# Kernel tuning notes

Hardware: AMD Instinct MI355X
Metric: run time of the kernel (lower is better)

The kernel has to match this reference:

```python
import jax, jax.numpy as jnp
import numpy as np

N = 200000
D = 128
B = 8
VS = 0.4
XMIN, YMIN, ZMIN = -50.0, -50.0, -5.0
NX, NY, NZ = 250, 250, 20
VXYZ = NX * NY * NZ
FILL = np.int32(2_000_000_000)  # > any real voxel key, so padded uniques sort last
BN_EPS = 1e-5


def _bn(x, g, b, m, v):
    # BatchNorm1d in eval mode with given running stats
    return (x - m) * jax.lax.rsqrt(v + BN_EPS) * g + b


def _leaky(x):
    return jnp.where(x >= 0, x, 0.1 * x)


def setup_inputs() -> dict:
    key = jax.random.key(0)
    ks = jax.random.split(key, 12)
    points_feature = jax.random.normal(ks[0], (N, D), jnp.float32)
    u = jax.random.uniform(ks[1], (N, 3), jnp.float32)
    lo = jnp.array([XMIN, YMIN, ZMIN], jnp.float32)
    ext = jnp.array([100.0, 100.0, 8.0], jnp.float32)
    points_center = lo + 0.001 + u * (ext - 0.002)  # strictly inside pc_range
    batch_idx = jax.random.randint(ks[2], (N,), 0, B, jnp.int32)
    foreground_mask = jax.random.randint(ks[3], (N,), 0, 2, jnp.int32).astype(bool)
    timestamp = jax.random.normal(ks[4], (B,), jnp.float32) * 0.1
    w_pf = jax.random.normal(ks[5], (3 * D, D), jnp.float32) / np.sqrt(3 * D)
    b_pf = jax.random.normal(ks[6], (D,), jnp.float32) * 0.01
    g_pf = jax.random.uniform(ks[7], (D,), jnp.float32) + 0.5
    be_pf = jax.random.normal(ks[8], (D,), jnp.float32) * 0.1
    m_pf = jax.random.normal(ks[9], (D,), jnp.float32) * 0.1
    v_pf = jax.random.uniform(ks[10], (D,), jnp.float32) + 0.5
    ks2 = jax.random.split(ks[11], 6)
    w_cp = jax.random.normal(ks2[0], (D, D), jnp.float32) / np.sqrt(D)
    b_cp = jax.random.normal(ks2[1], (D,), jnp.float32) * 0.01
    g_cp = jax.random.uniform(ks2[2], (D,), jnp.float32) + 0.5
    be_cp = jax.random.normal(ks2[3], (D,), jnp.float32) * 0.1
    m_cp = jax.random.normal(ks2[4], (D,), jnp.float32) * 0.1
    v_cp = jax.random.uniform(ks2[5], (D,), jnp.float32) + 0.5
    return dict(points_feature=points_feature, points_center=points_center,
                batch_idx=batch_idx, foreground_mask=foreground_mask,
                timestamp=timestamp,
                w_pf=w_pf, b_pf=b_pf, g_pf=g_pf, be_pf=be_pf, m_pf=m_pf, v_pf=v_pf,
                w_cp=w_cp, b_cp=b_cp, g_cp=g_cp, be_cp=be_cp, m_cp=m_cp, v_cp=v_cp)


def reference(points_feature, points_center, batch_idx, foreground_mask, timestamp,
              w_pf, b_pf, g_pf, be_pf, m_pf, v_pf,
              w_cp, b_cp, g_cp, be_cp, m_cp, v_cp):
    # NOTE: the original forward computes a time position embedding and then
    # overwrites it with zeros_like, so its net contribution is exactly zero.
    n = points_feature.shape[0]
    # voxelize point centers -> (b, xi, yi, zi) encoded as a single int key
    xi = jnp.floor((points_center[:, 0] - XMIN) / VS).astype(jnp.int32)
    yi = jnp.floor((points_center[:, 1] - YMIN) / VS).astype(jnp.int32)
    zi = jnp.floor((points_center[:, 2] - ZMIN) / VS).astype(jnp.int32)
    vkey = ((batch_idx.astype(jnp.int32) * NX + xi) * NY + yi) * NZ + zi
    # torch.unique(dim=0) sorts lexicographically == sorted scalar keys
    uk, inv = jnp.unique(vkey, return_inverse=True, size=n, fill_value=FILL)
    fgf = foreground_mask.astype(points_feature.dtype)
    # K = points_cluster_idx_fore.max() + 1 (number of foreground clusters)
    K = jnp.max(jnp.where(foreground_mask, inv, -1)) + 1
    # scatter_mean of foreground point features per cluster (empty -> 0)
    cnt = jax.ops.segment_sum(fgf, inv, num_segments=n)
    csum = jax.ops.segment_sum(points_feature * fgf[:, None], inv, num_segments=n)
    cmean = csum / jnp.maximum(cnt, 1.0)[:, None]
    proj = _leaky(_bn(cmean @ w_cp + b_cp, g_cp, be_cp, m_cp, v_cp))
    valid = jnp.arange(n) < K
    # cluster_feature_all: rows < K hold projected cluster features, rest are 0
    cfa = jnp.where(valid[:, None], proj, 0.0)
    # associate voxels: halve the batch id (agent pairing), re-unique
    akey = (uk // VXYZ // 2) * VXYZ + uk % VXYZ
    _, ainv = jnp.unique(akey, return_inverse=True, size=n, fill_value=FILL)
    # scatter_mean of cluster features over associate voxels (only valid clusters)
    acnt = jax.ops.segment_sum(valid.astype(points_feature.dtype), ainv, num_segments=n)
    asum = jax.ops.segment_sum(cfa, ainv, num_segments=n)
    amean = asum / jnp.maximum(acnt, 1.0)[:, None]
    pf_assoc = amean[ainv[inv]]   # gather per point via voxel -> associate id
    pf_clu = cfa[inv]             # gather per point cluster feature
    amask = (pf_clu - pf_assoc).sum(axis=1) > 0
    cat = jnp.concatenate([points_feature, pf_clu, pf_assoc], axis=1)
    h = _leaky(_bn(cat @ w_pf + b_pf, g_pf, be_pf, m_pf, v_pf))
    newf = jnp.where(amask[:, None], h, points_feature)
    # original early-returns points_feature if associate_mask.sum() <= 1
    return jnp.where(amask.sum() > 1, newf, points_feature)
```

## Files before the change

### kernel.cpp

```cpp
#include <hip/hip_runtime.h>

#define SCAN_BS 256
#define SCAN_IT 16
#define SCAN_CHUNK (SCAN_BS * SCAN_IT)
#define NVOX 10000000
#define NAVOX 5000000
#define NWORDS1 312500
#define NWORDS2 156250
#define VXYZK 1250000

__device__ __forceinline__ float leakyf(float x) { return x >= 0.0f ? x : 0.1f * x; }

__device__ __forceinline__ int fg_get(const void* fgp, int i, int mode) {
  return mode ? (((const unsigned char*)fgp)[i] != 0) : (((const int*)fgp)[i] != 0);
}

__global__ void k_vkey(const float* __restrict__ pc, const int* __restrict__ bidx,
                       const unsigned* __restrict__ fgw, int nw,
                       int* __restrict__ vkey, unsigned* __restrict__ bits,
                       int* __restrict__ c, int N) {
  int i = blockIdx.x * blockDim.x + threadIdx.x;
  if (i < nw && fgw[i] > 1u) atomicOr(&c[4], 1);
  if (i >= N) return;
  float x = pc[3 * i], y = pc[3 * i + 1], z = pc[3 * i + 2];
  int xi = (int)floorf((x - (-50.0f)) / 0.4f);
  int yi = (int)floorf((y - (-50.0f)) / 0.4f);
  int zi = (int)floorf((z - (-5.0f)) / 0.4f);
  xi = min(max(xi, 0), 249); yi = min(max(yi, 0), 249); zi = min(max(zi, 0), 19);
  int b = min(max(bidx[i], 0), 7);
  int key = ((b * 250 + xi) * 250 + yi) * 20 + zi;
  vkey[i] = key;
  atomicOr(&bits[key >> 5], 1u << (key & 31));
}

__global__ void k_scan_pop(const unsigned* __restrict__ bits, int nwords,
                           unsigned* __restrict__ wordpfx, unsigned* __restrict__ bsums) {
  __shared__ unsigned s[SCAN_BS];
  int tid = threadIdx.x;
  long base = (long)blockIdx.x * SCAN_CHUNK + (long)tid * SCAN_IT;
  unsigned v[SCAN_IT];
  unsigned tsum = 0;
#pragma unroll
  for (int j = 0; j < SCAN_IT; ++j) {
    long idx = base + j;
    v[j] = (idx < (long)nwords) ? (unsigned)__popc(bits[idx]) : 0u;
    tsum += v[j];
  }
  unsigned x = tsum;
  s[tid] = x;
  for (int off = 1; off < SCAN_BS; off <<= 1) {
    __syncthreads();
    unsigned y = (tid >= off) ? s[tid - off] : 0u;
    __syncthreads();
    x += y;
    s[tid] = x;
  }
  if (tid == SCAN_BS - 1) bsums[blockIdx.x] = x;
  unsigned run = x - tsum;
#pragma unroll
  for (int j = 0; j < SCAN_IT; ++j) {
    long idx = base + j;
    if (idx < (long)nwords) { wordpfx[idx] = run; run += v[j]; }
  }
}

__global__ void k_scan_sums(unsigned* __restrict__ data, int n, int* __restrict__ totalOut) {
  __shared__ unsigned s[SCAN_BS];
  int tid = threadIdx.x;
  int base = tid * SCAN_IT;
  unsigned v[SCAN_IT];
  unsigned tsum = 0;
#pragma unroll
  for (int j = 0; j < SCAN_IT; ++j) {
    int idx = base + j;
    v[j] = (idx < n) ? data[idx] : 0u;
    tsum += v[j];
  }
  unsigned x = tsum;
  s[tid] = x;
  for (int off = 1; off < SCAN_BS; off <<= 1) {
    __syncthreads();
    unsigned y = (tid >= off) ? s[tid - off] : 0u;
    __syncthreads();
    x += y;
    s[tid] = x;
  }
  if (tid == SCAN_BS - 1) *totalOut = (int)x;
  unsigned run = x - tsum;
#pragma unroll
  for (int j = 0; j < SCAN_IT; ++j) {
    int idx = base + j;
    if (idx < n) { data[idx] = run; run += v[j]; }
  }
}

__device__ __forceinline__ int rank_of(int key, const unsigned* bits,
                                       const unsigned* wordpfx, const unsigned* bsums) {
  int w = key >> 5, b = key & 31;
  return (int)(wordpfx[w] + bsums[w >> 12] + (unsigned)__popc(bits[w] & ((1u << b) - 1u)));
}

__global__ void k_inv_ukey(const int* __restrict__ vkey, const unsigned* __restrict__ bits,
                           const unsigned* __restrict__ wordpfx, const unsigned* __restrict__ bsums,
                           const void* __restrict__ fgp, int* __restrict__ inv,
                           int* __restrict__ ukey, int* __restrict__ c, int N) {
  int i = blockIdx.x * blockDim.x + threadIdx.x;
  bool valid = i < N;
  int mode = c[4];
  int r = 0;
  if (valid) {
    int k = vkey[i];
    r = rank_of(k, bits, wordpfx, bsums);
    inv[i] = r;
    ukey[r] = k;
  }
  int fgr = (valid && fg_get(fgp, i, mode)) ? r : -1;
  for (int off = 32; off > 0; off >>= 1) fgr = max(fgr, __shfl_down(fgr, off));
  if ((threadIdx.x & 63) == 0 && fgr >= 0) atomicMax(&c[2], fgr + 1);
}

__global__ void k_akey_mark(const int* __restrict__ ukey, int* __restrict__ akey,
                            unsigned* __restrict__ abits, const int* __restrict__ c, int N) {
  int r = blockIdx.x * blockDim.x + threadIdx.x;
  if (r >= N || r >= c[0]) return;
  int uk = ukey[r];
  int ak = (uk / VXYZK / 2) * VXYZK + uk % VXYZK;
  akey[r] = ak;
  atomicOr(&abits[ak >> 5], 1u << (ak & 31));
}

__global__ void k_ainv(const int* __restrict__ akey, const unsigned* __restrict__ abits,
                       const unsigned* __restrict__ awordpfx, const unsigned* __restrict__ bsums,
                       int* __restrict__ ainv, unsigned* __restrict__ gcnt,
                       const int* __restrict__ c, int N) {
  int r = blockIdx.x * blockDim.x + threadIdx.x;
  if (r >= N || r >= c[0]) return;
  int g = rank_of(akey[r], abits, awordpfx, bsums);
  ainv[r] = g;
  atomicAdd(&gcnt[g], 1u);
}

__global__ void k_build_lists(const int* __restrict__ ainv_u, const unsigned* __restrict__ gcnt,
                              int* __restrict__ mlist, int* __restrict__ nlist,
                              unsigned char* __restrict__ needp, int* __restrict__ c, int N) {
  int r = blockIdx.x * blockDim.x + threadIdx.x;
  if (r >= N || r >= c[0]) return;
  if (gcnt[ainv_u[r]] >= 2u) {
    int mp = atomicAdd(&c[5], 1);
    mlist[mp] = r;
    if (r < c[2]) {
      needp[r] = 1;
      int np = atomicAdd(&c[6], 1);
      nlist[np] = r;
    }
  }
}

__global__ void k_zero_filter(const int* __restrict__ mlist, const int* __restrict__ ainv_u,
                              const void* __restrict__ fgp, const int* __restrict__ inv,
                              const unsigned char* __restrict__ needp,
                              float* __restrict__ csum, float* __restrict__ asum,
                              float* __restrict__ cnt, int* __restrict__ clist,
                              int* __restrict__ c, int N) {
  int stride = gridDim.x * blockDim.x;
  int tid0 = blockIdx.x * blockDim.x + threadIdx.x;
  int K = c[2];
  int totalA = c[5] * 128;
  for (int idx = tid0; idx < totalA; idx += stride) {
    int r = mlist[idx >> 7];
    int d = idx & 127;
    asum[(size_t)ainv_u[r] * 128 + d] = 0.0f;
    if (r < K) csum[(size_t)r * 128 + d] = 0.0f;
  }
  int mode = c[4];
  for (int i = tid0; i < N; i += stride) {
    if (!fg_get(fgp, i, mode)) continue;
    int r = inv[i];
    if (!needp[r]) continue;
    atomicAdd(&cnt[r], 1.0f);
    int p = atomicAdd(&c[7], 1);
    clist[p] = i;
  }
}

__global__ void k_csum_accum(const float* __restrict__ pf, const int* __restrict__ clist,
                             const int* __restrict__ inv, float* __restrict__ csum,
                             const int* __restrict__ c) {
  int total = c[7] * 128;
  int stride = gridDim.x * blockDim.x;
  for (int idx = blockIdx.x * blockDim.x + threadIdx.x; idx < total; idx += stride) {
    int i = clist[idx >> 7];
    int d = idx & 127;
    atomicAdd(&csum[(size_t)inv[i] * 128 + d], pf[(size_t)i * 128 + d]);
  }
}

__global__ __launch_bounds__(128) void k_proj16(
    float* __restrict__ cs, const float* __restrict__ cnt, const int* __restrict__ nlist,
    const float* __restrict__ W, const float* __restrict__ bb,
    const float* __restrict__ gg, const float* __restrict__ be,
    const float* __restrict__ mm, const float* __restrict__ vv, const int* __restrict__ c) {
  int nc = c[6];
  int ntiles = (nc + 15) >> 4;
  __shared__ __align__(16) float tile[16][128];
  __shared__ int srow[16];
  int d = threadIdx.x;
  for (int tb = blockIdx.x; tb < ntiles; tb += gridDim.x) {
    int base = tb * 16;
    if (d < 16) srow[d] = (base + d < nc) ? nlist[base + d] : -1;
    __syncthreads();
    for (int p = 0; p < 16; ++p) {
      int r = srow[p];
      tile[p][d] = (r >= 0) ? cs[(size_t)r * 128 + d] / fmaxf(cnt[r], 1.0f) : 0.0f;
    }
    __syncthreads();
    float acc[16];
#pragma unroll
    for (int p = 0; p < 16; ++p) acc[p] = 0.0f;
    for (int k4 = 0; k4 < 32; ++k4) {
      float w0 = W[(4 * k4 + 0) * 128 + d];
      float w1 = W[(4 * k4 + 1) * 128 + d];
      float w2 = W[(4 * k4 + 2) * 128 + d];
      float w3 = W[(4 * k4 + 3) * 128 + d];
#pragma unroll
      for (int p = 0; p < 16; ++p) {
        float4 t4 = *(const float4*)&tile[p][4 * k4];
        acc[p] = fmaf(t4.x, w0, acc[p]);
        acc[p] = fmaf(t4.y, w1, acc[p]);
        acc[p] = fmaf(t4.z, w2, acc[p]);
        acc[p] = fmaf(t4.w, w3, acc[p]);
      }
    }
    float biasd = bb[d], scale = gg[d] / sqrtf(vv[d] + 1e-5f), md = mm[d], bed = be[d];
    for (int p = 0; p < 16; ++p) {
      int r = srow[p];
      if (r >= 0) {
        float pre = acc[p] + biasd;
        cs[(size_t)r * 128 + d] = leakyf((pre - md) * scale + bed);
      }
    }
    __syncthreads();
  }
}

__global__ void k_asum_accum(const float* __restrict__ cs, const int* __restrict__ nlist,
                             const int* __restrict__ ainv_u, float* __restrict__ asum,
                             float* __restrict__ acnt, const int* __restrict__ c) {
  int total = c[6] * 128;
  int stride = gridDim.x * blockDim.x;
  for (int idx = blockIdx.x * blockDim.x + threadIdx.x; idx < total; idx += stride) {
    int r = nlist[idx >> 7];
    int d = idx & 127;
    int g = ainv_u[r];
    atomicAdd(&asum[(size_t)g * 128 + d], cs[(size_t)r * 128 + d]);
    if (d == 0) atomicAdd(&acnt[g], 1.0f);
  }
}

__global__ void k_amask2(const float* __restrict__ cs, const float* __restrict__ asum,
                         const float* __restrict__ acnt, const int* __restrict__ ainv_u,
                         const int* __restrict__ mlist, const int* __restrict__ c,
                         unsigned* __restrict__ flag) {
  int mcount = c[5];
  int groups = gridDim.x * (blockDim.x >> 6);
  int j0 = blockIdx.x * (blockDim.x >> 6) + (threadIdx.x >> 6);
  int lane = threadIdx.x & 63;
  int K = c[2];
  for (int j = j0; j < mcount; j += groups) {
    int r = mlist[j];
    int g = ainv_u[r];
    float mc = fmaxf(acnt[g], 1.0f);
    bool valid = r < K;
    size_t rb = (size_t)r * 128, gb = (size_t)g * 128;
    float c0 = valid ? cs[rb + lane] : 0.0f;
    float c1 = valid ? cs[rb + 64 + lane] : 0.0f;
    float s = (c0 - asum[gb + lane] / mc) + (c1 - asum[gb + 64 + lane] / mc);
    for (int off = 32; off > 0; off >>= 1) s += __shfl_down(s, off);
    if (lane == 0) flag[r] = (s > 0.0f) ? 1u : 0u;
  }
}

__global__ void k_plist(const int* __restrict__ inv, const unsigned* __restrict__ flag,
                        int* __restrict__ plist, int* __restrict__ c, int N) {
  int i = blockIdx.x * blockDim.x + threadIdx.x;
  bool pred = (i < N) && (flag[inv[i]] != 0u);
  unsigned long long m = __ballot(pred);
  int lane = threadIdx.x & 63;
  int cnt = __popcll(m);
  int base = 0;
  if (lane == 0 && cnt) base = atomicAdd(&c[3], cnt);
  base = __shfl(base, 0);
  if (pred) plist[base + __popcll(m & ((1ull << lane) - 1ull))] = i;
}

__global__ __launch_bounds__(128) void k_fgemm(
    const float* __restrict__ pf, const float* __restrict__ cs,
    const float* __restrict__ asum, const float* __restrict__ acnt,
    const int* __restrict__ inv, const int* __restrict__ ainv_u,
    const int* __restrict__ plist, const int* __restrict__ c,
    const float* __restrict__ W, const float* __restrict__ bb,
    const float* __restrict__ gg, const float* __restrict__ be,
    const float* __restrict__ mm, const float* __restrict__ vv,
    float* __restrict__ out) {
  int pcnt = c[3];
  if (pcnt <= 1) return;
  int K = c[2];
  int ntiles = (pcnt + 15) >> 4;
  __shared__ __align__(16) float tile[16][384];
  __shared__ int si[16], sr[16], sg[16];
  __shared__ float smc[16];
  int t = threadIdx.x;
  for (int tb = blockIdx.x; tb < ntiles; tb += gridDim.x) {
    int base = tb * 16;
    if (t < 16) {
      int i = (base + t < pcnt) ? plist[base + t] : -1;
      si[t] = i;
      int r = (i >= 0) ? inv[i] : 0;
      sr[t] = r;
      int g = ainv_u[r];
      sg[t] = g;
      smc[t] = fmaxf(acnt[g], 1.0f);
    }
    __syncthreads();
    for (int e = t; e < 16 * 96; e += 128) {
      int p = e / 96, f4 = e % 96;
      int i = si[p];
      float4 v = make_float4(0.f, 0.f, 0.f, 0.f);
      if (i >= 0) {
        if (f4 < 32) {
          v = ((const float4*)pf)[(size_t)i * 32 + f4];
        } else if (f4 < 64) {
          int r = sr[p];
          if (r < K) v = ((const float4*)cs)[(size_t)r * 32 + (f4 - 32)];
        } else {
          float4 a = ((const float4*)asum)[(size_t)sg[p] * 32 + (f4 - 64)];
          float mc = smc[p];
          v = make_float4(a.x / mc, a.y / mc, a.z / mc, a.w / mc);
        }
      }
      *(float4*)&tile[p][f4 * 4] = v;
    }
    __syncthreads();
    float acc[16];
#pragma unroll
    for (int p = 0; p < 16; ++p) acc[p] = 0.0f;
    for (int k4 = 0; k4 < 96; ++k4) {
      float w0 = W[(4 * k4 + 0) * 128 + t];
      float w1 = W[(4 * k4 + 1) * 128 + t];
      float w2 = W[(4 * k4 + 2) * 128 + t];
      float w3 = W[(4 * k4 + 3) * 128 + t];
#pragma unroll
      for (int p = 0; p < 16; ++p) {
        float4 t4 = *(const float4*)&tile[p][4 * k4];
        acc[p] = fmaf(t4.x, w0, acc[p]);
        acc[p] = fmaf(t4.y, w1, acc[p]);
        acc[p] = fmaf(t4.z, w2, acc[p]);
        acc[p] = fmaf(t4.w, w3, acc[p]);
      }
    }
    float biasd = bb[t], scale = gg[t] / sqrtf(vv[t] + 1e-5f), md = mm[t], bed = be[t];
    for (int p = 0; p < 16; ++p) {
      int i = si[p];
      if (i >= 0) {
        float pre = acc[p] + biasd;
        out[(size_t)i * 128 + t] = leakyf((pre - md) * scale + bed);
      }
    }
    __syncthreads();
  }
}

extern "C" void kernel_launch(void* const* d_in, const int* in_sizes, int n_in,
                              void* d_out, int out_size, void* d_ws, size_t ws_size,
                              hipStream_t stream) {
  (void)n_in; (void)out_size; (void)ws_size;
  const float* pf   = (const float*)d_in[0];
  const float* pc   = (const float*)d_in[1];
  const int*   bidx = (const int*)d_in[2];
  const void*  fgp  = d_in[3];
  const float* Wpf  = (const float*)d_in[5];
  const float* bpf  = (const float*)d_in[6];
  const float* gpf  = (const float*)d_in[7];
  const float* bepf = (const float*)d_in[8];
  const float* mpf  = (const float*)d_in[9];
  const float* vpf  = (const float*)d_in[10];
  const float* Wcp  = (const float*)d_in[11];
  const float* bcp  = (const float*)d_in[12];
  const float* gcp  = (const float*)d_in[13];
  const float* becp = (const float*)d_in[14];
  const float* mcp  = (const float*)d_in[15];
  const float* vcp  = (const float*)d_in[16];
  float* out = (float*)d_out;
  int N = in_sizes[0] / 128;

  char* ws = (char*)d_ws;
  size_t o = 0;
  auto take = [&](size_t bytes) -> void* {
    void* p = ws + o;
    o += (bytes + 255) & ~(size_t)255;
    return p;
  };
  unsigned* bits   = (unsigned*)take((size_t)NWORDS1 * 4);
  unsigned* abits  = (unsigned*)take((size_t)NWORDS2 * 4);
  float* cnt       = (float*)take((size_t)N * 4);
  float* acnt      = (float*)take((size_t)N * 4);
  unsigned* flag   = (unsigned*)take((size_t)N * 4);
  unsigned* gcnt   = (unsigned*)take((size_t)N * 4);
  unsigned char* needp = (unsigned char*)take((size_t)N);
  int* ctr         = (int*)take(256);
  size_t zeroBytes = o;
  unsigned* wordpfx  = (unsigned*)take((size_t)NWORDS1 * 4);
  unsigned* awordpfx = (unsigned*)take((size_t)NWORDS2 * 4);
  unsigned* bsums1 = (unsigned*)take((size_t)4096 * 4);
  unsigned* bsums2 = (unsigned*)take((size_t)4096 * 4);
  int* vkey        = (int*)take((size_t)N * 4);
  int* inv         = (int*)take((size_t)N * 4);
  int* ukey        = (int*)take((size_t)N * 4);
  int* akey        = (int*)take((size_t)N * 4);
  int* ainv_u      = (int*)take((size_t)N * 4);
  int* nlist       = (int*)take((size_t)N * 4);
  int* clist       = (int*)take((size_t)N * 4);
  float* csum      = (float*)take((size_t)N * 128 * 4);
  float* asum      = (float*)take((size_t)N * 128 * 4);
  int* mlist = vkey;
  int* plist = akey;

  hipMemcpyAsync(out, pf, (size_t)N * 128 * sizeof(float),
                 hipMemcpyDeviceToDevice, stream);

  hipMemsetAsync(ws, 0, zeroBytes, stream);

  int nb = (N + 255) / 256;
  int nw = N / 4;
  k_vkey<<<nb, 256, 0, stream>>>(pc, bidx, (const unsigned*)fgp, nw, vkey, bits, ctr, N);

  int blk1 = (NWORDS1 + SCAN_CHUNK - 1) / SCAN_CHUNK;
  k_scan_pop<<<blk1, SCAN_BS, 0, stream>>>(bits, NWORDS1, wordpfx, bsums1);
  k_scan_sums<<<1, SCAN_BS, 0, stream>>>(bsums1, blk1, &ctr[0]);
  k_inv_ukey<<<nb, 256, 0, stream>>>(vkey, bits, wordpfx, bsums1, fgp, inv, ukey, ctr, N);

  k_akey_mark<<<nb, 256, 0, stream>>>(ukey, akey, abits, ctr, N);
  int blk2 = (NWORDS2 + SCAN_CHUNK - 1) / SCAN_CHUNK;
  k_scan_pop<<<blk2, SCAN_BS, 0, stream>>>(abits, NWORDS2, awordpfx, bsums2);
  k_scan_sums<<<1, SCAN_BS, 0, stream>>>(bsums2, blk2, &ctr[1]);
  k_ainv<<<nb, 256, 0, stream>>>(akey, abits, awordpfx, bsums2, ainv_u, gcnt, ctr, N);

  k_build_lists<<<nb, 256, 0, stream>>>(ainv_u, gcnt, mlist, nlist, needp, ctr, N);
  k_zero_filter<<<1024, 256, 0, stream>>>(mlist, ainv_u, fgp, inv, needp,
                                          csum, asum, cnt, clist, ctr, N);
  k_csum_accum<<<1024, 256, 0, stream>>>(pf, clist, inv, csum, ctr);
  k_proj16<<<512, 128, 0, stream>>>(csum, cnt, nlist, Wcp, bcp, gcp, becp, mcp, vcp, ctr);
  k_asum_accum<<<512, 256, 0, stream>>>(csum, nlist, ainv_u, asum, acnt, ctr);
  k_amask2<<<512, 256, 0, stream>>>(csum, asum, acnt, ainv_u, mlist, ctr, flag);

  k_plist<<<nb, 256, 0, stream>>>(inv, flag, plist, ctr, N);
  k_fgemm<<<1024, 128, 0, stream>>>(pf, csum, asum, acnt, inv, ainv_u, plist, ctr,
                                    Wpf, bpf, gpf, bepf, mpf, vpf, out);
}
```

Baseline: 467.6 us.

## Fuse all pipeline kernels into one cooperative persistent kernel with grid syncs

Replaces the chain of about fifteen kernel launches, the memset and the device-to-device memcpy with a single cooperative kernel. The phases are separated by grid-wide syncs, and the zeroing and feature copy are done by grid-stride loops inside it. This is meant to remove per-launch overhead and idle gaps between the many small dependent kernels. The cost is that every phase now runs on a fixed grid of at most 1024 blocks, grid-sync barriers are added, and the GEMM blocks move to 256 threads with 8 rows per thread-half.

```diff
diff --git a/kernel.cpp b/kernel.cpp
--- a/kernel.cpp
+++ b/kernel.cpp
@@ -1,4 +1,7 @@
 #include <hip/hip_runtime.h>
+#include <hip/hip_cooperative_groups.h>
+
+namespace cg = cooperative_groups;
 
 #define SCAN_BS 256
 #define SCAN_IT 16
@@ -8,6 +11,27 @@
 #define NWORDS1 312500
 #define NWORDS2 156250
 #define VXYZK 1250000
+#define BLK1 ((NWORDS1 + SCAN_CHUNK - 1) / SCAN_CHUNK)
+#define BLK2 ((NWORDS2 + SCAN_CHUNK - 1) / SCAN_CHUNK)
+
+struct Params {
+  const float* pf; const float* pc; const int* bidx; const void* fgp;
+  const float* Wpf; const float* bpf; const float* gpf; const float* bepf;
+  const float* mpf; const float* vpf;
+  const float* Wcp; const float* bcp; const float* gcp; const float* becp;
+  const float* mcp; const float* vcp;
+  float* out;
+  unsigned* bits; unsigned* abits; float* cnt; float* acnt;
+  unsigned* flag; unsigned* gcnt; unsigned char* needp; int* ctr;
+  unsigned* wordpfx; unsigned* awordpfx; unsigned* bsums1; unsigned* bsums2;
+  int* vkey;
+  int* inv; int* ukey;
+  int* akey;
+  int* ainv_u; int* nlist; int* clist;
+  float* csum; float* asum;
+  uint4* zbase; int zwords;
+  int N;
+};
 
 __device__ __forceinline__ float leakyf(float x) { return x >= 0.0f ? x : 0.1f * x; }
 
@@ -15,27 +39,19 @@
   return mode ? (((const unsigned char*)fgp)[i] != 0) : (((const int*)fgp)[i] != 0);
 }
 
-__global__ void k_vkey(const float* __restrict__ pc, const int* __restrict__ bidx,
-                       const unsigned* __restrict__ fgw, int nw,
-                       int* __restrict__ vkey, unsigned* __restrict__ bits,
-                       int* __restrict__ c, int N) {
-  int i = blockIdx.x * blockDim.x + threadIdx.x;
-  if (i < nw && fgw[i] > 1u) atomicOr(&c[4], 1);
-  if (i >= N) return;
-  float x = pc[3 * i], y = pc[3 * i + 1], z = pc[3 * i + 2];
-  int xi = (int)floorf((x - (-50.0f)) / 0.4f);
-  int yi = (int)floorf((y - (-50.0f)) / 0.4f);
-  int zi = (int)floorf((z - (-5.0f)) / 0.4f);
-  xi = min(max(xi, 0), 249); yi = min(max(yi, 0), 249); zi = min(max(zi, 0), 19);
-  int b = min(max(bidx[i], 0), 7);
-  int key = ((b * 250 + xi) * 250 + yi) * 20 + zi;
-  vkey[i] = key;
-  atomicOr(&bits[key >> 5], 1u << (key & 31));
-}
-
-__global__ void k_scan_pop(const unsigned* __restrict__ bits, int nwords,
-                           unsigned* __restrict__ wordpfx, unsigned* __restrict__ bsums) {
-  __shared__ unsigned s[SCAN_BS];
+__device__ __forceinline__ int rank_of(int key, const unsigned* bits,
+                                       const unsigned* wordpfx, const unsigned* bsums) {
+  int w = key >> 5, b = key & 31;
+  return (int)(wordpfx[w] + bsums[w >> 12] + (unsigned)__popc(bits[w] & ((1u << b) - 1u)));
+}
+
+struct ProjSM { float tile[16][128]; int srow[16]; };
+struct GemSM  { float tile[16][384]; int si[16]; int sr[16]; int sg[16]; float smc[16]; };
+union SM { unsigned scan[SCAN_BS]; ProjSM proj; GemSM gem; };
+
+__device__ void scan_pop_phase(const unsigned* __restrict__ bits, int nwords,
+                               unsigned* __restrict__ wordpfx, unsigned* __restrict__ bsums,
+                               unsigned* s) {
   int tid = threadIdx.x;
   long base = (long)blockIdx.x * SCAN_CHUNK + (long)tid * SCAN_IT;
   unsigned v[SCAN_IT];
@@ -64,8 +80,7 @@
   }
 }
 
-__global__ void k_scan_sums(unsigned* __restrict__ data, int n, int* __restrict__ totalOut) {
-  __shared__ unsigned s[SCAN_BS];
+__device__ void scan_sums_phase(unsigned* __restrict__ data, int n, int* totalOut, unsigned* s) {
   int tid = threadIdx.x;
   int base = tid * SCAN_IT;
   unsigned v[SCAN_IT];
@@ -94,279 +109,308 @@
   }
 }
 
-__device__ __forceinline__ int rank_of(int key, const unsigned* bits,
-                                       const unsigned* wordpfx, const unsigned* bsums) {
-  int w = key >> 5, b = key & 31;
-  return (int)(wordpfx[w] + bsums[w >> 12] + (unsigned)__popc(bits[w] & ((1u << b) - 1u)));
-}
-
-__global__ void k_inv_ukey(const int* __restrict__ vkey, const unsigned* __restrict__ bits,
-                           const unsigned* __restrict__ wordpfx, const unsigned* __restrict__ bsums,
-                           const void* __restrict__ fgp, int* __restrict__ inv,
-                           int* __restrict__ ukey, int* __restrict__ c, int N) {
-  int i = blockIdx.x * blockDim.x + threadIdx.x;
-  bool valid = i < N;
-  int mode = c[4];
-  int r = 0;
-  if (valid) {
-    int k = vkey[i];
-    r = rank_of(k, bits, wordpfx, bsums);
-    inv[i] = r;
-    ukey[r] = k;
-  }
-  int fgr = (valid && fg_get(fgp, i, mode)) ? r : -1;
-  for (int off = 32; off > 0; off >>= 1) fgr = max(fgr, __shfl_down(fgr, off));
-  if ((threadIdx.x & 63) == 0 && fgr >= 0) atomicMax(&c[2], fgr + 1);
-}
-
-__global__ void k_akey_mark(const int* __restrict__ ukey, int* __restrict__ akey,
-                            unsigned* __restrict__ abits, const int* __restrict__ c, int N) {
-  int r = blockIdx.x * blockDim.x + threadIdx.x;
-  if (r >= N || r >= c[0]) return;
-  int uk = ukey[r];
-  int ak = (uk / VXYZK / 2) * VXYZK + uk % VXYZK;
-  akey[r] = ak;
-  atomicOr(&abits[ak >> 5], 1u << (ak & 31));
-}
-
-__global__ void k_ainv(const int* __restrict__ akey, const unsigned* __restrict__ abits,
-                       const unsigned* __restrict__ awordpfx, const unsigned* __restrict__ bsums,
-                       int* __restrict__ ainv, unsigned* __restrict__ gcnt,
-                       const int* __restrict__ c, int N) {
-  int r = blockIdx.x * blockDim.x + threadIdx.x;
-  if (r >= N || r >= c[0]) return;
-  int g = rank_of(akey[r], abits, awordpfx, bsums);
-  ainv[r] = g;
-  atomicAdd(&gcnt[g], 1u);
-}
-
-__global__ void k_build_lists(const int* __restrict__ ainv_u, const unsigned* __restrict__ gcnt,
-                              int* __restrict__ mlist, int* __restrict__ nlist,
-                              unsigned char* __restrict__ needp, int* __restrict__ c, int N) {
-  int r = blockIdx.x * blockDim.x + threadIdx.x;
-  if (r >= N || r >= c[0]) return;
-  if (gcnt[ainv_u[r]] >= 2u) {
-    int mp = atomicAdd(&c[5], 1);
-    mlist[mp] = r;
-    if (r < c[2]) {
-      needp[r] = 1;
-      int np = atomicAdd(&c[6], 1);
-      nlist[np] = r;
-    }
-  }
-}
-
-__global__ void k_zero_filter(const int* __restrict__ mlist, const int* __restrict__ ainv_u,
-                              const void* __restrict__ fgp, const int* __restrict__ inv,
-                              const unsigned char* __restrict__ needp,
-                              float* __restrict__ csum, float* __restrict__ asum,
-                              float* __restrict__ cnt, int* __restrict__ clist,
-                              int* __restrict__ c, int N) {
-  int stride = gridDim.x * blockDim.x;
-  int tid0 = blockIdx.x * blockDim.x + threadIdx.x;
-  int K = c[2];
-  int totalA = c[5] * 128;
-  for (int idx = tid0; idx < totalA; idx += stride) {
-    int r = mlist[idx >> 7];
-    int d = idx & 127;
-    asum[(size_t)ainv_u[r] * 128 + d] = 0.0f;
-    if (r < K) csum[(size_t)r * 128 + d] = 0.0f;
-  }
-  int mode = c[4];
-  for (int i = tid0; i < N; i += stride) {
-    if (!fg_get(fgp, i, mode)) continue;
-    int r = inv[i];
-    if (!needp[r]) continue;
-    atomicAdd(&cnt[r], 1.0f);
-    int p = atomicAdd(&c[7], 1);
-    clist[p] = i;
-  }
-}
-
-__global__ void k_csum_accum(const float* __restrict__ pf, const int* __restrict__ clist,
-                             const int* __restrict__ inv, float* __restrict__ csum,
-                             const int* __restrict__ c) {
-  int total = c[7] * 128;
-  int stride = gridDim.x * blockDim.x;
-  for (int idx = blockIdx.x * blockDim.x + threadIdx.x; idx < total; idx += stride) {
-    int i = clist[idx >> 7];
-    int d = idx & 127;
-    atomicAdd(&csum[(size_t)inv[i] * 128 + d], pf[(size_t)i * 128 + d]);
-  }
-}
-
-__global__ __launch_bounds__(128) void k_proj16(
-    float* __restrict__ cs, const float* __restrict__ cnt, const int* __restrict__ nlist,
-    const float* __restrict__ W, const float* __restrict__ bb,
-    const float* __restrict__ gg, const float* __restrict__ be,
-    const float* __restrict__ mm, const float* __restrict__ vv, const int* __restrict__ c) {
-  int nc = c[6];
-  int ntiles = (nc + 15) >> 4;
-  __shared__ __align__(16) float tile[16][128];
-  __shared__ int srow[16];
-  int d = threadIdx.x;
-  for (int tb = blockIdx.x; tb < ntiles; tb += gridDim.x) {
-    int base = tb * 16;
-    if (d < 16) srow[d] = (base + d < nc) ? nlist[base + d] : -1;
-    __syncthreads();
-    for (int p = 0; p < 16; ++p) {
-      int r = srow[p];
-      tile[p][d] = (r >= 0) ? cs[(size_t)r * 128 + d] / fmaxf(cnt[r], 1.0f) : 0.0f;
-    }
-    __syncthreads();
-    float acc[16];
-#pragma unroll
-    for (int p = 0; p < 16; ++p) acc[p] = 0.0f;
-    for (int k4 = 0; k4 < 32; ++k4) {
-      float w0 = W[(4 * k4 + 0) * 128 + d];
-      float w1 = W[(4 * k4 + 1) * 128 + d];
-      float w2 = W[(4 * k4 + 2) * 128 + d];
-      float w3 = W[(4 * k4 + 3) * 128 + d];
-#pragma unroll
-      for (int p = 0; p < 16; ++p) {
-        float4 t4 = *(const float4*)&tile[p][4 * k4];
-        acc[p] = fmaf(t4.x, w0, acc[p]);
-        acc[p] = fmaf(t4.y, w1, acc[p]);
-        acc[p] = fmaf(t4.z, w2, acc[p]);
-        acc[p] = fmaf(t4.w, w3, acc[p]);
-      }
-    }
-    float biasd = bb[d], scale = gg[d] / sqrtf(vv[d] + 1e-5f), md = mm[d], bed = be[d];
-    for (int p = 0; p < 16; ++p) {
-      int r = srow[p];
-      if (r >= 0) {
-        float pre = acc[p] + biasd;
-        cs[(size_t)r * 128 + d] = leakyf((pre - md) * scale + bed);
-      }
-    }
-    __syncthreads();
-  }
-}
-
-__global__ void k_asum_accum(const float* __restrict__ cs, const int* __restrict__ nlist,
-                             const int* __restrict__ ainv_u, float* __restrict__ asum,
-                             float* __restrict__ acnt, const int* __restrict__ c) {
-  int total = c[6] * 128;
-  int stride = gridDim.x * blockDim.x;
-  for (int idx = blockIdx.x * blockDim.x + threadIdx.x; idx < total; idx += stride) {
-    int r = nlist[idx >> 7];
-    int d = idx & 127;
-    int g = ainv_u[r];
-    atomicAdd(&asum[(size_t)g * 128 + d], cs[(size_t)r * 128 + d]);
-    if (d == 0) atomicAdd(&acnt[g], 1.0f);
-  }
-}
-
-__global__ void k_amask2(const float* __restrict__ cs, const float* __restrict__ asum,
-                         const float* __restrict__ acnt, const int* __restrict__ ainv_u,
-                         const int* __restrict__ mlist, const int* __restrict__ c,
-                         unsigned* __restrict__ flag) {
-  int mcount = c[5];
-  int groups = gridDim.x * (blockDim.x >> 6);
-  int j0 = blockIdx.x * (blockDim.x >> 6) + (threadIdx.x >> 6);
-  int lane = threadIdx.x & 63;
-  int K = c[2];
-  for (int j = j0; j < mcount; j += groups) {
-    int r = mlist[j];
-    int g = ainv_u[r];
-    float mc = fmaxf(acnt[g], 1.0f);
-    bool valid = r < K;
-    size_t rb = (size_t)r * 128, gb = (size_t)g * 128;
-    float c0 = valid ? cs[rb + lane] : 0.0f;
-    float c1 = valid ? cs[rb + 64 + lane] : 0.0f;
-    float s = (c0 - asum[gb + lane] / mc) + (c1 - asum[gb + 64 + lane] / mc);
-    for (int off = 32; off > 0; off >>= 1) s += __shfl_down(s, off);
-    if (lane == 0) flag[r] = (s > 0.0f) ? 1u : 0u;
-  }
-}
-
-__global__ void k_plist(const int* __restrict__ inv, const unsigned* __restrict__ flag,
-                        int* __restrict__ plist, int* __restrict__ c, int N) {
-  int i = blockIdx.x * blockDim.x + threadIdx.x;
-  bool pred = (i < N) && (flag[inv[i]] != 0u);
-  unsigned long long m = __ballot(pred);
-  int lane = threadIdx.x & 63;
-  int cnt = __popcll(m);
-  int base = 0;
-  if (lane == 0 && cnt) base = atomicAdd(&c[3], cnt);
-  base = __shfl(base, 0);
-  if (pred) plist[base + __popcll(m & ((1ull << lane) - 1ull))] = i;
-}
-
-__global__ __launch_bounds__(128) void k_fgemm(
-    const float* __restrict__ pf, const float* __restrict__ cs,
-    const float* __restrict__ asum, const float* __restrict__ acnt,
-    const int* __restrict__ inv, const int* __restrict__ ainv_u,
-    const int* __restrict__ plist, const int* __restrict__ c,
-    const float* __restrict__ W, const float* __restrict__ bb,
-    const float* __restrict__ gg, const float* __restrict__ be,
-    const float* __restrict__ mm, const float* __restrict__ vv,
-    float* __restrict__ out) {
-  int pcnt = c[3];
-  if (pcnt <= 1) return;
-  int K = c[2];
-  int ntiles = (pcnt + 15) >> 4;
-  __shared__ __align__(16) float tile[16][384];
-  __shared__ int si[16], sr[16], sg[16];
-  __shared__ float smc[16];
-  int t = threadIdx.x;
-  for (int tb = blockIdx.x; tb < ntiles; tb += gridDim.x) {
-    int base = tb * 16;
-    if (t < 16) {
-      int i = (base + t < pcnt) ? plist[base + t] : -1;
-      si[t] = i;
-      int r = (i >= 0) ? inv[i] : 0;
-      sr[t] = r;
-      int g = ainv_u[r];
-      sg[t] = g;
-      smc[t] = fmaxf(acnt[g], 1.0f);
-    }
-    __syncthreads();
-    for (int e = t; e < 16 * 96; e += 128) {
-      int p = e / 96, f4 = e % 96;
-      int i = si[p];
-      float4 v = make_float4(0.f, 0.f, 0.f, 0.f);
-      if (i >= 0) {
-        if (f4 < 32) {
-          v = ((const float4*)pf)[(size_t)i * 32 + f4];
-        } else if (f4 < 64) {
-          int r = sr[p];
-          if (r < K) v = ((const float4*)cs)[(size_t)r * 32 + (f4 - 32)];
-        } else {
-          float4 a = ((const float4*)asum)[(size_t)sg[p] * 32 + (f4 - 64)];
-          float mc = smc[p];
-          v = make_float4(a.x / mc, a.y / mc, a.z / mc, a.w / mc);
-        }
-      }
-      *(float4*)&tile[p][f4 * 4] = v;
-    }
-    __syncthreads();
-    float acc[16];
-#pragma unroll
-    for (int p = 0; p < 16; ++p) acc[p] = 0.0f;
-    for (int k4 = 0; k4 < 96; ++k4) {
-      float w0 = W[(4 * k4 + 0) * 128 + t];
-      float w1 = W[(4 * k4 + 1) * 128 + t];
-      float w2 = W[(4 * k4 + 2) * 128 + t];
-      float w3 = W[(4 * k4 + 3) * 128 + t];
-#pragma unroll
-      for (int p = 0; p < 16; ++p) {
-        float4 t4 = *(const float4*)&tile[p][4 * k4];
-        acc[p] = fmaf(t4.x, w0, acc[p]);
-        acc[p] = fmaf(t4.y, w1, acc[p]);
-        acc[p] = fmaf(t4.z, w2, acc[p]);
-        acc[p] = fmaf(t4.w, w3, acc[p]);
-      }
-    }
-    float biasd = bb[t], scale = gg[t] / sqrtf(vv[t] + 1e-5f), md = mm[t], bed = be[t];
-    for (int p = 0; p < 16; ++p) {
-      int i = si[p];
-      if (i >= 0) {
-        float pre = acc[p] + biasd;
-        out[(size_t)i * 128 + t] = leakyf((pre - md) * scale + bed);
-      }
-    }
-    __syncthreads();
+__global__ void k_fused(Params p) {
+  cg::grid_group grid = cg::this_grid();
+  __shared__ __align__(16) SM sm;
+  const int tid = threadIdx.x;
+  const int bid = blockIdx.x;
+  const int nth = gridDim.x * blockDim.x;
+  const int gtid = bid * blockDim.x + tid;
+  const int N = p.N;
+  volatile int* cv = p.ctr;
+
+  {
+    uint4 z = make_uint4(0u, 0u, 0u, 0u);
+    for (int w = gtid; w < p.zwords; w += nth) p.zbase[w] = z;
+  }
+  grid.sync();
+
+  {
+    const int nw = N / 4;
+    const unsigned* fgw = (const unsigned*)p.fgp;
+    for (int i = gtid; i < N; i += nth) {
+      if (i < nw && fgw[i] > 1u) atomicOr(&p.ctr[4], 1);
+      float x = p.pc[3 * i], y = p.pc[3 * i + 1], z = p.pc[3 * i + 2];
+      int xi = (int)floorf((x - (-50.0f)) / 0.4f);
+      int yi = (int)floorf((y - (-50.0f)) / 0.4f);
+      int zi = (int)floorf((z - (-5.0f)) / 0.4f);
+      xi = min(max(xi, 0), 249); yi = min(max(yi, 0), 249); zi = min(max(zi, 0), 19);
+      int b = min(max(p.bidx[i], 0), 7);
+      int key = ((b * 250 + xi) * 250 + yi) * 20 + zi;
+      p.vkey[i] = key;
+      atomicOr(&p.bits[key >> 5], 1u << (key & 31));
+    }
+    const float4* s4 = (const float4*)p.pf;
+    float4* d4 = (float4*)p.out;
+    int n4 = N * 32;
+    int e = gtid;
+    for (; e + 3 * nth < n4; e += 4 * nth) {
+      float4 v0 = s4[e], v1 = s4[e + nth], v2 = s4[e + 2 * nth], v3 = s4[e + 3 * nth];
+      d4[e] = v0; d4[e + nth] = v1; d4[e + 2 * nth] = v2; d4[e + 3 * nth] = v3;
+    }
+    for (; e < n4; e += nth) d4[e] = s4[e];
+  }
+  grid.sync();
+
+  if (bid < BLK1) scan_pop_phase(p.bits, NWORDS1, p.wordpfx, p.bsums1, sm.scan);
+  grid.sync();
+  if (bid == 0) scan_sums_phase(p.bsums1, BLK1, &p.ctr[0], sm.scan);
+  grid.sync();
+
+  {
+    int mode = cv[4];
+    int iters = (N + nth - 1) / nth;
+    for (int it = 0; it < iters; ++it) {
+      int i = it * nth + gtid;
+      bool valid = i < N;
+      int r = 0;
+      if (valid) {
+        int k = p.vkey[i];
+        r = rank_of(k, p.bits, p.wordpfx, p.bsums1);
+        p.inv[i] = r;
+        p.ukey[r] = k;
+      }
+      int fgr = (valid && fg_get(p.fgp, i, mode)) ? r : -1;
+      for (int off = 32; off > 0; off >>= 1) fgr = max(fgr, __shfl_down(fgr, off));
+      if ((tid & 63) == 0 && fgr >= 0) atomicMax(&p.ctr[2], fgr + 1);
+    }
+  }
+  grid.sync();
+
+  {
+    int U = cv[0];
+    for (int r = gtid; r < U; r += nth) {
+      int uk = p.ukey[r];
+      int ak = (uk / VXYZK / 2) * VXYZK + uk % VXYZK;
+      p.akey[r] = ak;
+      atomicOr(&p.abits[ak >> 5], 1u << (ak & 31));
+    }
+  }
+  grid.sync();
+
+  if (bid < BLK2) scan_pop_phase(p.abits, NWORDS2, p.awordpfx, p.bsums2, sm.scan);
+  grid.sync();
+  if (bid == 0) scan_sums_phase(p.bsums2, BLK2, &p.ctr[1], sm.scan);
+  grid.sync();
+
+  {
+    int U = cv[0];
+    for (int r = gtid; r < U; r += nth) {
+      int g = rank_of(p.akey[r], p.abits, p.awordpfx, p.bsums2);
+      p.ainv_u[r] = g;
+      atomicAdd(&p.gcnt[g], 1u);
+    }
+  }
+  grid.sync();
+
+  {
+    int U = cv[0];
+    int K = cv[2];
+    for (int r = gtid; r < U; r += nth) {
+      if (p.gcnt[p.ainv_u[r]] >= 2u) {
+        int mp = atomicAdd(&p.ctr[5], 1);
+        p.vkey[mp] = r;
+        if (r < K) {
+          p.needp[r] = 1;
+          int np = atomicAdd(&p.ctr[6], 1);
+          p.nlist[np] = r;
+        }
+      }
+    }
+  }
+  grid.sync();
+
+  {
+    int K = cv[2];
+    int mcount = cv[5];
+    int mode = cv[4];
+    int totalA = mcount * 128;
+    for (int idx = gtid; idx < totalA; idx += nth) {
+      int r = p.vkey[idx >> 7];
+      int d = idx & 127;
+      p.asum[(size_t)p.ainv_u[r] * 128 + d] = 0.0f;
+      if (r < K) p.csum[(size_t)r * 128 + d] = 0.0f;
+    }
+    for (int i = gtid; i < N; i += nth) {
+      if (!fg_get(p.fgp, i, mode)) continue;
+      int r = p.inv[i];
+      if (!p.needp[r]) continue;
+      atomicAdd(&p.cnt[r], 1.0f);
+      int q = atomicAdd(&p.ctr[7], 1);
+      p.clist[q] = i;
+    }
+  }
+  grid.sync();
+
+  {
+    int total = cv[7] * 128;
+    for (int idx = gtid; idx < total; idx += nth) {
+      int i = p.clist[idx >> 7];
+      int d = idx & 127;
+      atomicAdd(&p.csum[(size_t)p.inv[i] * 128 + d], p.pf[(size_t)i * 128 + d]);
+    }
+  }
+  grid.sync();
+
+  {
+    int nc = cv[6];
+    int ntiles = (nc + 15) >> 4;
+    int d = tid & 127, h = tid >> 7;
+    for (int tb = bid; tb < ntiles; tb += gridDim.x) {
+      int base = tb * 16;
+      if (tid < 16) sm.proj.srow[tid] = (base + tid < nc) ? p.nlist[base + tid] : -1;
+      __syncthreads();
+      for (int q = h; q < 16; q += 2) {
+        int r = sm.proj.srow[q];
+        sm.proj.tile[q][d] = (r >= 0) ? p.csum[(size_t)r * 128 + d] / fmaxf(p.cnt[r], 1.0f) : 0.0f;
+      }
+      __syncthreads();
+      float acc[8];
+#pragma unroll
+      for (int q = 0; q < 8; ++q) acc[q] = 0.0f;
+      for (int k4 = 0; k4 < 32; ++k4) {
+        float w0 = p.Wcp[(4 * k4 + 0) * 128 + d];
+        float w1 = p.Wcp[(4 * k4 + 1) * 128 + d];
+        float w2 = p.Wcp[(4 * k4 + 2) * 128 + d];
+        float w3 = p.Wcp[(4 * k4 + 3) * 128 + d];
+#pragma unroll
+        for (int q = 0; q < 8; ++q) {
+          float4 t4 = *(const float4*)&sm.proj.tile[h * 8 + q][4 * k4];
+          acc[q] = fmaf(t4.x, w0, acc[q]);
+          acc[q] = fmaf(t4.y, w1, acc[q]);
+          acc[q] = fmaf(t4.z, w2, acc[q]);
+          acc[q] = fmaf(t4.w, w3, acc[q]);
+        }
+      }
+      float biasd = p.bcp[d], scale = p.gcp[d] / sqrtf(p.vcp[d] + 1e-5f);
+      float md = p.mcp[d], bed = p.becp[d];
+      for (int q = 0; q < 8; ++q) {
+        int r = sm.proj.srow[h * 8 + q];
+        if (r >= 0) {
+          float pre = acc[q] + biasd;
+          p.csum[(size_t)r * 128 + d] = leakyf((pre - md) * scale + bed);
+        }
+      }
+      __syncthreads();
+    }
+  }
+  grid.sync();
+
+  {
+    int total = cv[6] * 128;
+    for (int idx = gtid; idx < total; idx += nth) {
+      int r = p.nlist[idx >> 7];
+      int d = idx & 127;
+      int g = p.ainv_u[r];
+      atomicAdd(&p.asum[(size_t)g * 128 + d], p.csum[(size_t)r * 128 + d]);
+      if (d == 0) atomicAdd(&p.acnt[g], 1.0f);
+    }
+  }
+  grid.sync();
+
+  {
+    int mcount = cv[5];
+    int K = cv[2];
+    int groups = gridDim.x * (blockDim.x >> 6);
+    int j0 = bid * (blockDim.x >> 6) + (tid >> 6);
+    int lane = tid & 63;
+    for (int j = j0; j < mcount; j += groups) {
+      int r = p.vkey[j];
+      int g = p.ainv_u[r];
+      float mc = fmaxf(p.acnt[g], 1.0f);
+      bool valid = r < K;
+      size_t rb = (size_t)r * 128, gb = (size_t)g * 128;
+      float c0 = valid ? p.csum[rb + lane] : 0.0f;
+      float c1 = valid ? p.csum[rb + 64 + lane] : 0.0f;
+      float s = (c0 - p.asum[gb + lane] / mc) + (c1 - p.asum[gb + 64 + lane] / mc);
+      for (int off = 32; off > 0; off >>= 1) s += __shfl_down(s, off);
+      if (lane == 0) p.flag[r] = (s > 0.0f) ? 1u : 0u;
+    }
+  }
+  grid.sync();
+
+  {
+    int iters = (N + nth - 1) / nth;
+    int lane = tid & 63;
+    for (int it = 0; it < iters; ++it) {
+      int i = it * nth + gtid;
+      bool pred = (i < N) && (p.flag[p.inv[i]] != 0u);
+      unsigned long long m = __ballot(pred);
+      int cnt = __popcll(m);
+      int base = 0;
+      if (lane == 0 && cnt) base = atomicAdd(&p.ctr[3], cnt);
+      base = __shfl(base, 0);
+      if (pred) p.akey[base + __popcll(m & ((1ull << lane) - 1ull))] = i;
+    }
+  }
+  grid.sync();
+
+  {
+    int pcnt = cv[3];
+    if (pcnt > 1) {
+      int K = cv[2];
+      int ntiles = (pcnt + 15) >> 4;
+      int d = tid & 127, h = tid >> 7;
+      for (int tb = bid; tb < ntiles; tb += gridDim.x) {
+        int base = tb * 16;
+        if (tid < 16) {
+          int i = (base + tid < pcnt) ? p.akey[base + tid] : -1;
+          sm.gem.si[tid] = i;
+          int r = (i >= 0) ? p.inv[i] : 0;
+          sm.gem.sr[tid] = r;
+          int g = p.ainv_u[r];
+          sm.gem.sg[tid] = g;
+          sm.gem.smc[tid] = fmaxf(p.acnt[g], 1.0f);
+        }
+        __syncthreads();
+        for (int e = tid; e < 16 * 96; e += 256) {
+          int q = e / 96, f4 = e % 96;
+          int i = sm.gem.si[q];
+          float4 v = make_float4(0.f, 0.f, 0.f, 0.f);
+          if (i >= 0) {
+            if (f4 < 32) {
+              v = ((const float4*)p.pf)[(size_t)i * 32 + f4];
+            } else if (f4 < 64) {
+              int r = sm.gem.sr[q];
+              if (r < K) v = ((const float4*)p.csum)[(size_t)r * 32 + (f4 - 32)];
+            } else {
+              float4 a = ((const float4*)p.asum)[(size_t)sm.gem.sg[q] * 32 + (f4 - 64)];
+              float mc = sm.gem.smc[q];
+              v = make_float4(a.x / mc, a.y / mc, a.z / mc, a.w / mc);
+            }
+          }
+          *(float4*)&sm.gem.tile[q][f4 * 4] = v;
+        }
+        __syncthreads();
+        float acc[8];
+#pragma unroll
+        for (int q = 0; q < 8; ++q) acc[q] = 0.0f;
+        for (int k4 = 0; k4 < 96; ++k4) {
+          float w0 = p.Wpf[(4 * k4 + 0) * 128 + d];
+          float w1 = p.Wpf[(4 * k4 + 1) * 128 + d];
+          float w2 = p.Wpf[(4 * k4 + 2) * 128 + d];
+          float w3 = p.Wpf[(4 * k4 + 3) * 128 + d];
+#pragma unroll
+          for (int q = 0; q < 8; ++q) {
+            float4 t4 = *(const float4*)&sm.gem.tile[h * 8 + q][4 * k4];
+            acc[q] = fmaf(t4.x, w0, acc[q]);
+            acc[q] = fmaf(t4.y, w1, acc[q]);
+            acc[q] = fmaf(t4.z, w2, acc[q]);
+            acc[q] = fmaf(t4.w, w3, acc[q]);
+          }
+        }
+        float biasd = p.bpf[d], scale = p.gpf[d] / sqrtf(p.vpf[d] + 1e-5f);
+        float md = p.mpf[d], bed = p.bepf[d];
+        for (int q = 0; q < 8; ++q) {
+          int i = sm.gem.si[h * 8 + q];
+          if (i >= 0) {
+            float pre = acc[q] + biasd;
+            p.out[(size_t)i * 128 + d] = leakyf((pre - md) * scale + bed);
+          }
+        }
+        __syncthreads();
+      }
+    }
   }
 }
 
@@ -374,24 +418,26 @@
                               void* d_out, int out_size, void* d_ws, size_t ws_size,
                               hipStream_t stream) {
   (void)n_in; (void)out_size; (void)ws_size;
-  const float* pf   = (const float*)d_in[0];
-  const float* pc   = (const float*)d_in[1];
-  const int*   bidx = (const int*)d_in[2];
-  const void*  fgp  = d_in[3];
-  const float* Wpf  = (const float*)d_in[5];
-  const float* bpf  = (const float*)d_in[6];
-  const float* gpf  = (const float*)d_in[7];
-  const float* bepf = (const float*)d_in[8];
-  const float* mpf  = (const float*)d_in[9];
-  const float* vpf  = (const float*)d_in[10];
-  const float* Wcp  = (const float*)d_in[11];
-  const float* bcp  = (const float*)d_in[12];
-  const float* gcp  = (const float*)d_in[13];
-  const float* becp = (const float*)d_in[14];
-  const float* mcp  = (const float*)d_in[15];
-  const float* vcp  = (const float*)d_in[16];
-  float* out = (float*)d_out;
+  Params prm;
+  prm.pf   = (const float*)d_in[0];
+  prm.pc   = (const float*)d_in[1];
+  prm.bidx = (const int*)d_in[2];
+  prm.fgp  = d_in[3];
+  prm.Wpf  = (const float*)d_in[5];
+  prm.bpf  = (const float*)d_in[6];
+  prm.gpf  = (const float*)d_in[7];
+  prm.bepf = (const float*)d_in[8];
+  prm.mpf  = (const float*)d_in[9];
+  prm.vpf  = (const float*)d_in[10];
+  prm.Wcp  = (const float*)d_in[11];
+  prm.bcp  = (const float*)d_in[12];
+  prm.gcp  = (const float*)d_in[13];
+  prm.becp = (const float*)d_in[14];
+  prm.mcp  = (const float*)d_in[15];
+  prm.vcp  = (const float*)d_in[16];
+  prm.out  = (float*)d_out;
   int N = in_sizes[0] / 128;
+  prm.N = N;
 
   char* ws = (char*)d_ws;
   size_t o = 0;
@@ -400,60 +446,37 @@
     o += (bytes + 255) & ~(size_t)255;
     return p;
   };
-  unsigned* bits   = (unsigned*)take((size_t)NWORDS1 * 4);
-  unsigned* abits  = (unsigned*)take((size_t)NWORDS2 * 4);
-  float* cnt       = (float*)take((size_t)N * 4);
-  float* acnt      = (float*)take((size_t)N * 4);
-  unsigned* flag   = (unsigned*)take((size_t)N * 4);
-  unsigned* gcnt   = (unsigned*)take((size_t)N * 4);
-  unsigned char* needp = (unsigned char*)take((size_t)N);
-  int* ctr         = (int*)take(256);
+  prm.bits  = (unsigned*)take((size_t)NWORDS1 * 4);
+  prm.abits = (unsigned*)take((size_t)NWORDS2 * 4);
+  prm.cnt   = (float*)take((size_t)N * 4);
+  prm.acnt  = (float*)take((size_t)N * 4);
+  prm.flag  = (unsigned*)take((size_t)N * 4);
+  prm.gcnt  = (unsigned*)take((size_t)N * 4);
+  prm.needp = (unsigned char*)take((size_t)N);
+  prm.ctr   = (int*)take(256);
   size_t zeroBytes = o;
-  unsigned* wordpfx  = (unsigned*)take((size_t)NWORDS1 * 4);
-  unsigned* awordpfx = (unsigned*)take((size_t)NWORDS2 * 4);
-  unsigned* bsums1 = (unsigned*)take((size_t)4096 * 4);
-  unsigned* bsums2 = (unsigned*)take((size_t)4096 * 4);
-  int* vkey        = (int*)take((size_t)N * 4);
-  int* inv         = (int*)take((size_t)N * 4);
-  int* ukey        = (int*)take((size_t)N * 4);
-  int* akey        = (int*)take((size_t)N * 4);
-  int* ainv_u      = (int*)take((size_t)N * 4);
-  int* nlist       = (int*)take((size_t)N * 4);
-  int* clist       = (int*)take((size_t)N * 4);
-  float* csum      = (float*)take((size_t)N * 128 * 4);
-  float* asum      = (float*)take((size_t)N * 128 * 4);
-  int* mlist = vkey;
-  int* plist = akey;
-
-  hipMemcpyAsync(out, pf, (size_t)N * 128 * sizeof(float),
-                 hipMemcpyDeviceToDevice, stream);
-
-  hipMemsetAsync(ws, 0, zeroBytes, stream);
-
-  int nb = (N + 255) / 256;
-  int nw = N / 4;
-  k_vkey<<<nb, 256, 0, stream>>>(pc, bidx, (const unsigned*)fgp, nw, vkey, bits, ctr, N);
-
-  int blk1 = (NWORDS1 + SCAN_CHUNK - 1) / SCAN_CHUNK;
-  k_scan_pop<<<blk1, SCAN_BS, 0, stream>>>(bits, NWORDS1, wordpfx, bsums1);
-  k_scan_sums<<<1, SCAN_BS, 0, stream>>>(bsums1, blk1, &ctr[0]);
-  k_inv_ukey<<<nb, 256, 0, stream>>>(vkey, bits, wordpfx, bsums1, fgp, inv, ukey, ctr, N);
-
-  k_akey_mark<<<nb, 256, 0, stream>>>(ukey, akey, abits, ctr, N);
-  int blk2 = (NWORDS2 + SCAN_CHUNK - 1) / SCAN_CHUNK;
-  k_scan_pop<<<blk2, SCAN_BS, 0, stream>>>(abits, NWORDS2, awordpfx, bsums2);
-  k_scan_sums<<<1, SCAN_BS, 0, stream>>>(bsums2, blk2, &ctr[1]);
-  k_ainv<<<nb, 256, 0, stream>>>(akey, abits, awordpfx, bsums2, ainv_u, gcnt, ctr, N);
-
-  k_build_lists<<<nb, 256, 0, stream>>>(ainv_u, gcnt, mlist, nlist, needp, ctr, N);
-  k_zero_filter<<<1024, 256, 0, stream>>>(mlist, ainv_u, fgp, inv, needp,
-                                          csum, asum, cnt, clist, ctr, N);
-  k_csum_accum<<<1024, 256, 0, stream>>>(pf, clist, inv, csum, ctr);
-  k_proj16<<<512, 128, 0, stream>>>(csum, cnt, nlist, Wcp, bcp, gcp, becp, mcp, vcp, ctr);
-  k_asum_accum<<<512, 256, 0, stream>>>(csum, nlist, ainv_u, asum, acnt, ctr);
-  k_amask2<<<512, 256, 0, stream>>>(csum, asum, acnt, ainv_u, mlist, ctr, flag);
-
-  k_plist<<<nb, 256, 0, stream>>>(inv, flag, plist, ctr, N);
-  k_fgemm<<<1024, 128, 0, stream>>>(pf, csum, asum, acnt, inv, ainv_u, plist, ctr,
-                                    Wpf, bpf, gpf, bepf, mpf, vpf, out);
-}
+  prm.wordpfx  = (unsigned*)take((size_t)NWORDS1 * 4);
+  prm.awordpfx = (unsigned*)take((size_t)NWORDS2 * 4);
+  prm.bsums1   = (unsigned*)take((size_t)4096 * 4);
+  prm.bsums2   = (unsigned*)take((size_t)4096 * 4);
+  prm.vkey     = (int*)take((size_t)N * 4);
+  prm.inv      = (int*)take((size_t)N * 4);
+  prm.ukey     = (int*)take((size_t)N * 4);
+  prm.akey     = (int*)take((size_t)N * 4);
+  prm.ainv_u   = (int*)take((size_t)N * 4);
+  prm.nlist    = (int*)take((size_t)N * 4);
+  prm.clist    = (int*)take((size_t)N * 4);
+  prm.csum     = (float*)take((size_t)N * 128 * 4);
+  prm.asum     = (float*)take((size_t)N * 128 * 4);
+  prm.zbase  = (uint4*)ws;
+  prm.zwords = (int)(zeroBytes / 16);
+
+  int mb = 0;
+  hipOccupancyMaxActiveBlocksPerMultiprocessor(&mb, (const void*)k_fused, 256, 0);
+  if (mb < 1) mb = 1;
+  int G = mb * 256;
+  if (G > 1024) G = 1024;
+
+  void* args[] = { (void*)&prm };
+  hipLaunchCooperativeKernel((const void*)k_fused, dim3(G), dim3(256), args, 0, stream);
+}
```

New measurement: 1.284 ms. 175% more time.
